# Kernel tuning notes

Hardware: AMD Instinct MI355X
Metric: run time of the kernel (lower is better)

Reference implementation:

```python
import jax, jax.numpy as jnp
import numpy as np

B, N, C, H, OUT = 4, 1024, 1024, 16, 1024
HEAD_DIM_INIT = C // H          # 64, used for scale per __init__
SCALE = HEAD_DIM_INIT ** -0.5
HD = 2 * C // H                 # 128, actual per-head dim after the reshape


def setup_inputs() -> dict:
    key = jax.random.key(0)
    k0, k1, k2, k3 = jax.random.split(key, 4)
    return {
        "x": jax.random.normal(k0, (B, N, C), jnp.float32),
        "context": jax.random.normal(k1, (B, N, C), jnp.float32),
        "w_qkv": jax.random.normal(k2, (3 * C, C), jnp.float32) / np.sqrt(C).astype(np.float32),
        "w_proj": jax.random.normal(k3, (OUT, C), jnp.float32) / np.sqrt(C).astype(np.float32),
        "b_proj": jnp.zeros((OUT,), jnp.float32),
    }


def reference(x, context, w_qkv, w_proj, b_proj):
    b, n, c = x.shape
    hd = 2 * c // H
    xc = jnp.concatenate([x, context], axis=1)                 # [B, 2N, C]
    qkv = jnp.einsum('bsc,dc->bsd', xc, w_qkv)                 # [B, 2N, 3C]
    # faithful to torch: reshape(B, N, 3, H, 2C/H) then permute(2,0,3,1,4)
    qkv = qkv.reshape(b, n, 3, H, hd).transpose(2, 0, 3, 1, 4)  # [3, B, H, N, HD]
    q, k, v = qkv[0], qkv[1], qkv[2]
    attn = jax.nn.softmax(jnp.einsum('bhqd,bhkd->bhqk', q, k) * SCALE, axis=-1)  # [B,H,N,N]
    o = jnp.einsum('bhqk,bhkd->bhqd', attn, v)                 # [B, H, N, HD]
    o = o.transpose(0, 2, 1, 3).reshape(b, 2 * n, c)           # [B, 2N, C]
    out = jnp.einsum('bsc,oc->bso', o, w_proj) + b_proj        # [B, 2N, OUT]
    return out, attn
```

## Files before the change

### kernel.cpp

```cpp
#include <hip/hip_runtime.h>
#include <stdint.h>

typedef short bf16x8 __attribute__((ext_vector_type(8)));
typedef short s16x4 __attribute__((ext_vector_type(4)));
typedef unsigned short us8 __attribute__((ext_vector_type(8)));
typedef float f32x4 __attribute__((ext_vector_type(4)));
typedef unsigned short u16;
typedef unsigned int u32;

__device__ __forceinline__ u16 f2bf(float f) {
    u32 u = __float_as_uint(f);
    return (u16)((u + 0x7FFFu + ((u >> 16) & 1u)) >> 16);
}
__device__ __forceinline__ float bf2f(u16 h) { return __uint_as_float(((u32)h) << 16); }

__device__ __forceinline__ u32 cvtpk(float lo, float hi) {
    u32 r;
    asm("v_cvt_pk_bf16_f32 %0, %1, %2" : "=v"(r) : "v"(lo), "v"(hi));
    return r;
}

typedef __attribute__((address_space(3))) unsigned int lds_uint;
typedef const __attribute__((address_space(1))) unsigned int glb_uint;
__device__ __forceinline__ void gld16(const void* g, void* l) {
    __builtin_amdgcn_global_load_lds((glb_uint*)g, (lds_uint*)l, 16, 0, 0);
}

#define VWAIT(n) asm volatile("s_waitcnt vmcnt(" #n ") lgkmcnt(0)" ::: "memory")
#define LWAIT    asm volatile("s_waitcnt lgkmcnt(0)" ::: "memory")
#define BARRIER  do { __builtin_amdgcn_s_barrier(); __builtin_amdgcn_sched_barrier(0); } while (0)


__device__ __forceinline__ void gld_p128x32(const u16* __restrict__ g, int64_t stride,
                                            u16* lds, int w, int lane) {
#pragma unroll
    for (int i = 0; i < 2; ++i) {
        const int grp = w * 2 + i;
        const int row = grp * 16 + (lane >> 2);
        const int sl = (lane & 3) ^ ((row >> 1) & 3);
        gld16(g + (int64_t)row * stride + (sl << 3), &lds[grp * 512]);
    }
}
__device__ __forceinline__ int idx128x32(int row, int gk) {
    return row * 32 + ((gk ^ ((row >> 1) & 3)) << 3);
}

__device__ __forceinline__ void gld_t32x128(const u16* __restrict__ g, int64_t stride,
                                            u16* lds, int w, int lane) {
#pragma unroll
    for (int i = 0; i < 2; ++i) {
        const int gg = w * 2 + i;
        const int row = gg * 4 + (lane >> 4);
        const int gs = (lane & 15) ^ (row & 7);
        gld16(g + (int64_t)row * stride + (gs << 3), &lds[gg * 512]);
    }
}
__device__ __forceinline__ void gld_t64x128(const u16* __restrict__ g, int64_t stride,
                                            u16* lds, int w, int lane) {
#pragma unroll
    for (int i = 0; i < 4; ++i) {
        const int gg = w * 4 + i;
        const int row = gg * 4 + (lane >> 4);
        const int gs = (lane & 15) ^ (row & 7);
        gld16(g + (int64_t)row * stride + (gs << 3), &lds[gg * 512]);
    }
}
__device__ __forceinline__ int idxT(int row, int gk) {
    return row * 128 + ((gk ^ (row & 7)) << 3);
}

__device__ __forceinline__ void gld_v128x64(const u16* __restrict__ g, int64_t stride,
                                            u16* lds, int w, int lane) {
#pragma unroll
    for (int i = 0; i < 4; ++i) {
        const int seg = w * 4 + i;
        const int row = seg * 8 + (lane >> 3);
        const int gs = (lane & 7) ^ (row & 7);
        gld16(g + (int64_t)row * stride + (gs << 3), &lds[seg * 512]);
    }
}
__device__ __forceinline__ int idxV(int row, int g3) {
    return row * 64 + ((g3 ^ (row & 7)) << 3);
}

__global__ void k0_all(const float* __restrict__ wqkv, const float* __restrict__ x,
                       const float* __restrict__ ctx, const float* __restrict__ wproj,
                       u16* __restrict__ Wh, u16* __restrict__ Xh,
                       u16* __restrict__ Phw) {
    const int gid = blockIdx.x;
    const float* src; u16* dst; int mode; int lg;
    if (gid < 1536)      { src = wqkv;  dst = Wh;  mode = 0; lg = gid; }
    else if (gid < 3584) { src = x;     dst = Xh;  mode = 1; lg = gid - 1536; }
    else if (gid < 5632) { src = ctx;   dst = Xh;  mode = 2; lg = gid - 3584; }
    else                 { src = wproj; dst = Phw; mode = 0; lg = gid - 5632; }
    const int64_t base = ((int64_t)lg * 256 + threadIdx.x) * 8;
    const int row = (int)(base >> 10), col = (int)(base & 1023);
    int orow = row;
    if (mode == 1) orow = row + ((row >> 10) << 10);
    else if (mode == 2) orow = row + (((row >> 10) + 1) << 10);
    const float4* sp = reinterpret_cast<const float4*>(src + base);
    float4 a = sp[0], b = sp[1];
    float v[8] = {a.x, a.y, a.z, a.w, b.x, b.y, b.z, b.w};
    us8 hh;
#pragma unroll
    for (int j = 0; j < 8; ++j) hh[j] = f2bf(v[j]);
    *reinterpret_cast<us8*>(&dst[(int64_t)orow * 1024 + col]) = hh;
}

template<bool ISK4>
__global__ __launch_bounds__(512, 1) void gemm8p(const u16* __restrict__ Ap,
                                                 const u16* __restrict__ Bp,
                                                 const float* __restrict__ bias,
                                                 u16* __restrict__ outh,
                                                 float* __restrict__ outf) {
    __shared__ u16 L[3][2][8192];
    const int tid = threadIdx.x, lane = tid & 63;
    const int w = tid >> 6, wm = w >> 2, wn = w & 3;
    const int rl = lane & 15, gk = lane >> 4, r4 = gk << 2;
    const int n0 = blockIdx.x << 7, m0 = blockIdx.y << 8;
    const u16* Ab = Ap + (int64_t)m0 * 1024;
    const u16* Bb = Bp + (int64_t)n0 * 1024;
    const int srow0 = tid >> 3, scol = tid & 7;
    f32x4 acc[2][4][2] = {};
    bf16x8 afr[4][2];

#define STAGE1(X, KT) do { if ((X) >= 0 && (KT) < 16) {                          \
    const u16* _b = (((X) < 2) ? (Ab + (int64_t)((X) * 128) * 1024) : Bb)        \
                    + (KT) * 64;                                                 \
    u16* _l = &L[((X) < 0) ? 0 : (X)][(KT) & 1][0];                              \
    _Pragma("unroll") for (int _j = 0; _j < 2; ++_j) {                           \
        const int _r = _j * 64 + srow0;                                          \
        const int _g = scol ^ (_r & 7);                                          \
        gld16(_b + (int64_t)_r * 1024 + _g * 8, &_l[_r * 64 + scol * 8]);        \
    } } } while (0)

#define RDF(X, PAR, ROW, KHGK)                                                   \
    (*reinterpret_cast<const bf16x8*>(                                           \
        &L[(X)][(PAR)][(ROW) * 64 + (((KHGK) ^ ((ROW) & 7)) << 3)]))

#define PHASE(QM, QN, PAR, STX, STKT, WMODE) do {                                \
    STAGE1(STX, STKT);                                                           \
    if ((WMODE) == 1) { VWAIT(4); } else if ((WMODE) == 2) { VWAIT(0); }         \
    __builtin_amdgcn_s_barrier(); __builtin_amdgcn_sched_barrier(0);             \
    if ((QN) == 0) {                                                             \
        _Pragma("unroll") for (int _mf = 0; _mf < 4; ++_mf) {                    \
            afr[_mf][0] = RDF(QM, PAR, wm * 64 + _mf * 16 + rl, gk);             \
            afr[_mf][1] = RDF(QM, PAR, wm * 64 + _mf * 16 + rl, 4 + gk);         \
        } }                                                                      \
    bf16x8 _b0 = RDF(2, PAR, (QN) * 64 + wn * 16 + rl, gk);                      \
    bf16x8 _b1 = RDF(2, PAR, (QN) * 64 + wn * 16 + rl, 4 + gk);                  \
    LWAIT; __builtin_amdgcn_sched_barrier(0);                                    \
    __builtin_amdgcn_s_setprio(1);                                               \
    _Pragma("unroll") for (int _mf = 0; _mf < 4; ++_mf) {                        \
        acc[QM][_mf][QN] = __builtin_amdgcn_mfma_f32_16x16x32_bf16(              \
            afr[_mf][0], _b0, acc[QM][_mf][QN], 0, 0, 0);                        \
        acc[QM][_mf][QN] = __builtin_amdgcn_mfma_f32_16x16x32_bf16(              \
            afr[_mf][1], _b1, acc[QM][_mf][QN], 0, 0, 0);                        \
    }                                                                            \
    __builtin_amdgcn_s_setprio(0);                                               \
    __builtin_amdgcn_s_barrier(); __builtin_amdgcn_sched_barrier(0);             \
} while (0)

    STAGE1(0, 0); STAGE1(1, 0); STAGE1(2, 0); STAGE1(0, 1);
    for (int i = 0; i < 8; ++i) {
        const int t = 2 * i;
        PHASE(0, 0, 0, 1, t + 1, 1);
        PHASE(0, 1, 0, 2, t + 1, 0);
        PHASE(1, 0, 0, 0, t + 2, 0);
        PHASE(1, 1, 0, -1, 0, 0);
        PHASE(0, 0, 1, 1, t + 2, (i == 7) ? 2 : 1);
        PHASE(0, 1, 1, 2, t + 2, 0);
        PHASE(1, 0, 1, 0, t + 3, 0);
        PHASE(1, 1, 1, -1, 0, 0);
    }
#undef PHASE
#undef RDF
#undef STAGE1
#pragma unroll
    for (int qm = 0; qm < 2; ++qm)
#pragma unroll
        for (int mf = 0; mf < 4; ++mf)
#pragma unroll
            for (int qn = 0; qn < 2; ++qn)
#pragma unroll
                for (int j = 0; j < 4; ++j) {
                    const int row = m0 + qm * 128 + wm * 64 + mf * 16 + r4 + j;
                    const int col = n0 + qn * 64 + wn * 16 + rl;
                    if (ISK4)
                        outf[(int64_t)row * 1024 + col] = acc[qm][mf][qn][j] + bias[col];
                    else
                        outh[(int64_t)row * 3072 + col] = f2bf(acc[qm][mf][qn][j]);
                }
}

__global__ __launch_bounds__(256, 2) void k0v_vt(const u16* __restrict__ Qh,
                                                 u16* __restrict__ Vt) {
    __shared__ u16 T[128][144];
    const int tid = threadIdx.x;
    const int z = blockIdx.y, b = z >> 4, h = z & 15;
    const int kt = blockIdx.x;
    const int c0v = (h < 8) ? (1024 + h * 128) : (2048 + (h - 8) * 128);
    const u16* Vbase = Qh + ((int64_t)b * 2048 + 1) * 3072 + c0v;
    const int row = tid >> 1, e0 = (tid & 1) << 6;
    const u16* src = Vbase + (int64_t)(kt * 128 + row) * 6144 + e0;
#pragma unroll
    for (int i = 0; i < 8; ++i) {
        us8 v = *reinterpret_cast<const us8*>(src + i * 8);
#pragma unroll
        for (int j = 0; j < 8; ++j) T[e0 + i * 8 + j][row] = v[j];
    }
    __syncthreads();
    const int e = tid >> 1, k0 = (tid & 1) << 6;
    u16* dst = Vt + ((int64_t)z << 17) + (int64_t)e * 1024 + kt * 128 + k0;
#pragma unroll
    for (int i = 0; i < 8; ++i)
        *reinterpret_cast<us8*>(dst + i * 8) = *reinterpret_cast<const us8*>(&T[e][k0 + i * 8]);
}

__global__ __launch_bounds__(256, 2) void k23_fused(const u16* __restrict__ Qh,
                                                    const u16* __restrict__ Vt,
                                                    float* __restrict__ attn,
                                                    u16* __restrict__ Obf) {
    __shared__ u16 LQ[4096];
    __shared__ u16 LKV[3][8192];
    __shared__ u16 Ph[32 * 72];
    __shared__ float pS[4][32];
    __shared__ float rowInv[32];
    const int tid = threadIdx.x, lane = tid & 63, w = tid >> 6;
    const u32 wgid = blockIdx.x;
    const int xcd = wgid & 7, t0 = wgid >> 3;
    const int mt = t0 & 31, z = ((t0 >> 5) << 3) + xcd;
    const int b = z >> 4, h = z & 15;
    const int m0 = mt << 5;
    const u16* Qbase = Qh + ((int64_t)b * 2048 + 2 * m0) * 3072 + h * 128;
    const int pk  = (h < 8) ? 0 : 1;
    const int c0k = (h < 8) ? (2048 + h * 128) : ((h - 8) * 128);
    const u16* Kbase = Qh + ((int64_t)b * 2048 + pk) * 3072 + c0k;
    const u16* Vtz = Vt + ((int64_t)z << 17);
    float* attnZ = attn + ((int64_t)z << 20) + (int64_t)m0 * 1024;
    const int rl = lane & 15, gk = lane >> 4;
    const int r4 = gk << 2;
    const int sm = w & 1, sn = w >> 1;
    gld_t32x128(Qbase, 6144, LQ, w, lane);
    gld_t64x128(Kbase,             6144, LKV[0], w, lane);
    gld_t64x128(Kbase + 64 * 6144, 6144, LKV[1], w, lane);
    u32 pk0[32], pk1[32];
    float ssum0 = 0.f, ssum1 = 0.f;
#pragma unroll
    for (int t = 0; t < 16; ++t) {
        if (t == 15) { VWAIT(0); } else { VWAIT(4); }
        BARRIER;
        if (t < 14)
            gld_t64x128(Kbase + (int64_t)(t + 2) * 64 * 6144, 6144, LKV[(t + 2) % 3], w, lane);
        f32x4 s0 = {}, s1 = {};
#pragma unroll
        for (int ks = 0; ks < 4; ++ks) {
            bf16x8 kf = *reinterpret_cast<const bf16x8*>(&LKV[t % 3][idxT(w * 16 + rl, ks * 4 + gk)]);
            bf16x8 q0 = *reinterpret_cast<const bf16x8*>(&LQ[idxT(rl, ks * 4 + gk)]);
            bf16x8 q1 = *reinterpret_cast<const bf16x8*>(&LQ[idxT(16 + rl, ks * 4 + gk)]);
            s0 = __builtin_amdgcn_mfma_f32_16x16x32_bf16(kf, q0, s0, 0, 0, 0);
            s1 = __builtin_amdgcn_mfma_f32_16x16x32_bf16(kf, q1, s1, 0, 0, 0);
        }
        float p0[4], p1[4];
#pragma unroll
        for (int j = 0; j < 4; ++j) {
            p0[j] = __expf(s0[j] * 0.125f); ssum0 += p0[j];
            p1[j] = __expf(s1[j] * 0.125f); ssum1 += p1[j];
        }
        pk0[2 * t]     = cvtpk(p0[0], p0[1]);
        pk1[2 * t]     = cvtpk(p0[2], p0[3]);
        pk0[2 * t + 1] = cvtpk(p1[0], p1[1]);
        pk1[2 * t + 1] = cvtpk(p1[2], p1[3]);
    }
    ssum0 += __shfl_xor(ssum0, 16); ssum0 += __shfl_xor(ssum0, 32);
    ssum1 += __shfl_xor(ssum1, 16); ssum1 += __shfl_xor(ssum1, 32);
    if (lane < 16) { pS[w][lane] = ssum0; pS[w][16 + lane] = ssum1; }
    LWAIT; BARRIER;
    gld_v128x64(Vtz,      1024, LKV[0], w, lane);
    gld_v128x64(Vtz + 64, 1024, LKV[1], w, lane);
    if (tid < 32)
        rowInv[tid] = 1.0f / (pS[0][tid] + pS[1][tid] + pS[2][tid] + pS[3][tid]);
    LWAIT; BARRIER;
    const float Iq0 = rowInv[rl], Iq1 = rowInv[16 + rl];
    float IqO[4];
#pragma unroll
    for (int j = 0; j < 4; ++j) IqO[j] = rowInv[sm * 16 + r4 + j];
    f32x4 po[4] = {};
#pragma unroll
    for (int t = 0; t < 16; ++t) {
        if (t == 0)       { VWAIT(4); }
        else if (t == 15) { VWAIT(2); }
        else              { VWAIT(6); }
        BARRIER;
        if (t < 14)
            gld_v128x64(Vtz + (t + 2) * 64, 1024, LKV[(t + 2) % 3], w, lane);
        const u32 a0 = pk0[2 * t], a1 = pk1[2 * t];
        const u32 b0 = pk0[2 * t + 1], b1 = pk1[2 * t + 1];
        *reinterpret_cast<uint2*>(&Ph[rl * 72 + w * 16 + r4])        = make_uint2(a0, a1);
        *reinterpret_cast<uint2*>(&Ph[(16 + rl) * 72 + w * 16 + r4]) = make_uint2(b0, b1);
        *reinterpret_cast<float4*>(&attnZ[(int64_t)rl * 1024 + t * 64 + w * 16 + r4])
            = make_float4(__uint_as_float(a0 << 16) * Iq0,
                          __uint_as_float(a0 & 0xFFFF0000u) * Iq0,
                          __uint_as_float(a1 << 16) * Iq0,
                          __uint_as_float(a1 & 0xFFFF0000u) * Iq0);
        *reinterpret_cast<float4*>(&attnZ[(int64_t)(16 + rl) * 1024 + t * 64 + w * 16 + r4])
            = make_float4(__uint_as_float(b0 << 16) * Iq1,
                          __uint_as_float(b0 & 0xFFFF0000u) * Iq1,
                          __uint_as_float(b1 << 16) * Iq1,
                          __uint_as_float(b1 & 0xFFFF0000u) * Iq1);
        LWAIT; BARRIER;
        bf16x8 pa0 = *reinterpret_cast<const bf16x8*>(&Ph[(sm * 16 + rl) * 72 + gk * 8]);
        bf16x8 pa1 = *reinterpret_cast<const bf16x8*>(&Ph[(sm * 16 + rl) * 72 + 32 + gk * 8]);
#pragma unroll
        for (int n = 0; n < 4; ++n) {
            bf16x8 bv0 = *reinterpret_cast<const bf16x8*>(&LKV[t % 3][idxV(sn * 64 + n * 16 + rl, gk)]);
            bf16x8 bv1 = *reinterpret_cast<const bf16x8*>(&LKV[t % 3][idxV(sn * 64 + n * 16 + rl, 4 + gk)]);
            po[n] = __builtin_amdgcn_mfma_f32_16x16x32_bf16(pa0, bv0, po[n], 0, 0, 0);
            po[n] = __builtin_amdgcn_mfma_f32_16x16x32_bf16(pa1, bv1, po[n], 0, 0, 0);
        }
    }
    const int poh = h >> 3, cb2 = (h & 7) << 7;
#pragma unroll
    for (int n = 0; n < 4; ++n)
#pragma unroll
        for (int j = 0; j < 4; ++j) {
            const int qrow = m0 + sm * 16 + r4 + j;
            Obf[((int64_t)b * 2048 + 2 * qrow + poh) * 1024
                + cb2 + sn * 64 + n * 16 + rl] = f2bf(po[n][j] * IqO[j]);
        }
}

extern "C" void kernel_launch(void* const* d_in, const int* in_sizes, int n_in,
                              void* d_out, int out_size, void* d_ws, size_t ws_size,
                              hipStream_t stream) {
    const float* x     = (const float*)d_in[0];
    const float* ctx   = (const float*)d_in[1];
    const float* wqkv  = (const float*)d_in[2];
    const float* wproj = (const float*)d_in[3];
    const float* bias  = (const float*)d_in[4];
    float* out  = (float*)d_out;
    float* attn = out + 8388608;

    u16* Qh  = (u16*)d_ws;
    u16* Vt  = Qh + 25165824;
    u16* Wh  = Vt + 8388608;
    u16* Phw = Wh + 3145728;
    u16* Obf = Phw + 1048576;

    u16* Xh = (u16*)attn;

    k0_all        <<<dim3(6144),   256, 0, stream>>>(wqkv, x, ctx, wproj, Wh, Xh, Phw);
    gemm8p<false> <<<dim3(24, 32), 512, 0, stream>>>(Xh, Wh, nullptr, Qh, nullptr);
    k0v_vt        <<<dim3(8, 64),  256, 0, stream>>>(Qh, Vt);
    k23_fused     <<<dim3(2048),   256, 0, stream>>>(Qh, Vt, attn, Obf);
    gemm8p<true>  <<<dim3(8, 32),  512, 0, stream>>>(Obf, Phw, bias, nullptr, out);
}
```

Measured before the change: 231.8 us.

## Double attention query tile to 64 rows with 8-wave workgroups sharing K/V tiles

The fused attention kernel now processes 64 query rows per workgroup with 512 threads (8 waves) instead of 32 rows with 4 waves, halving the grid. Each K and V tile staged in LDS is reused by twice as many query rows, which cuts global/L2 traffic for K and V, and the per-wave async load count and wait counts are adjusted to match. In exchange, LDS use per workgroup grows and launch_bounds(512,4) may constrain registers, which matters because of the 64 packed probability registers each thread keeps.

```diff
diff --git a/kernel.cpp b/kernel.cpp
--- a/kernel.cpp
+++ b/kernel.cpp
@@ -2,7 +2,6 @@
 #include <stdint.h>
 
 typedef short bf16x8 __attribute__((ext_vector_type(8)));
-typedef short s16x4 __attribute__((ext_vector_type(4)));
 typedef unsigned short us8 __attribute__((ext_vector_type(8)));
 typedef float f32x4 __attribute__((ext_vector_type(4)));
 typedef unsigned short u16;
@@ -12,7 +11,6 @@
     u32 u = __float_as_uint(f);
     return (u16)((u + 0x7FFFu + ((u >> 16) & 1u)) >> 16);
 }
-__device__ __forceinline__ float bf2f(u16 h) { return __uint_as_float(((u32)h) << 16); }
 
 __device__ __forceinline__ u32 cvtpk(float lo, float hi) {
     u32 r;
@@ -31,22 +29,8 @@
 #define BARRIER  do { __builtin_amdgcn_s_barrier(); __builtin_amdgcn_sched_barrier(0); } while (0)
 
 
-__device__ __forceinline__ void gld_p128x32(const u16* __restrict__ g, int64_t stride,
-                                            u16* lds, int w, int lane) {
-#pragma unroll
-    for (int i = 0; i < 2; ++i) {
-        const int grp = w * 2 + i;
-        const int row = grp * 16 + (lane >> 2);
-        const int sl = (lane & 3) ^ ((row >> 1) & 3);
-        gld16(g + (int64_t)row * stride + (sl << 3), &lds[grp * 512]);
-    }
-}
-__device__ __forceinline__ int idx128x32(int row, int gk) {
-    return row * 32 + ((gk ^ ((row >> 1) & 3)) << 3);
-}
-
-__device__ __forceinline__ void gld_t32x128(const u16* __restrict__ g, int64_t stride,
-                                            u16* lds, int w, int lane) {
+__device__ __forceinline__ void gld8_t64x128(const u16* __restrict__ g, int64_t stride,
+                                             u16* lds, int w, int lane) {
 #pragma unroll
     for (int i = 0; i < 2; ++i) {
         const int gg = w * 2 + i;
@@ -55,25 +39,15 @@
         gld16(g + (int64_t)row * stride + (gs << 3), &lds[gg * 512]);
     }
 }
-__device__ __forceinline__ void gld_t64x128(const u16* __restrict__ g, int64_t stride,
-                                            u16* lds, int w, int lane) {
-#pragma unroll
-    for (int i = 0; i < 4; ++i) {
-        const int gg = w * 4 + i;
-        const int row = gg * 4 + (lane >> 4);
-        const int gs = (lane & 15) ^ (row & 7);
-        gld16(g + (int64_t)row * stride + (gs << 3), &lds[gg * 512]);
-    }
-}
 __device__ __forceinline__ int idxT(int row, int gk) {
     return row * 128 + ((gk ^ (row & 7)) << 3);
 }
 
-__device__ __forceinline__ void gld_v128x64(const u16* __restrict__ g, int64_t stride,
-                                            u16* lds, int w, int lane) {
-#pragma unroll
-    for (int i = 0; i < 4; ++i) {
-        const int seg = w * 4 + i;
+__device__ __forceinline__ void gld8_v128x64(const u16* __restrict__ g, int64_t stride,
+                                             u16* lds, int w, int lane) {
+#pragma unroll
+    for (int i = 0; i < 2; ++i) {
+        const int seg = w * 2 + i;
         const int row = seg * 8 + (lane >> 3);
         const int gs = (lane & 7) ^ (row & 7);
         gld16(g + (int64_t)row * stride + (gs << 3), &lds[seg * 512]);
@@ -217,47 +191,47 @@
         *reinterpret_cast<us8*>(dst + i * 8) = *reinterpret_cast<const us8*>(&T[e][k0 + i * 8]);
 }
 
-__global__ __launch_bounds__(256, 2) void k23_fused(const u16* __restrict__ Qh,
+__global__ __launch_bounds__(512, 4) void k23_fused(const u16* __restrict__ Qh,
                                                     const u16* __restrict__ Vt,
                                                     float* __restrict__ attn,
                                                     u16* __restrict__ Obf) {
-    __shared__ u16 LQ[4096];
+    __shared__ u16 LQ[8192];
     __shared__ u16 LKV[3][8192];
-    __shared__ u16 Ph[32 * 72];
-    __shared__ float pS[4][32];
-    __shared__ float rowInv[32];
+    __shared__ u16 Ph[64 * 72];
+    __shared__ float pS[8][32];
+    __shared__ float rowInv[64];
     const int tid = threadIdx.x, lane = tid & 63, w = tid >> 6;
     const u32 wgid = blockIdx.x;
     const int xcd = wgid & 7, t0 = wgid >> 3;
-    const int mt = t0 & 31, z = ((t0 >> 5) << 3) + xcd;
+    const int mt = t0 & 15, z = ((t0 >> 4) << 3) + xcd;
     const int b = z >> 4, h = z & 15;
-    const int m0 = mt << 5;
+    const int m0 = mt << 6;
+    const int kt = w & 3, qh = w >> 2;
+    const int qq = w & 3, sv = w >> 2;
+    const int rl = lane & 15, gk = lane >> 4, r4 = gk << 2;
     const u16* Qbase = Qh + ((int64_t)b * 2048 + 2 * m0) * 3072 + h * 128;
     const int pk  = (h < 8) ? 0 : 1;
     const int c0k = (h < 8) ? (2048 + h * 128) : ((h - 8) * 128);
     const u16* Kbase = Qh + ((int64_t)b * 2048 + pk) * 3072 + c0k;
     const u16* Vtz = Vt + ((int64_t)z << 17);
     float* attnZ = attn + ((int64_t)z << 20) + (int64_t)m0 * 1024;
-    const int rl = lane & 15, gk = lane >> 4;
-    const int r4 = gk << 2;
-    const int sm = w & 1, sn = w >> 1;
-    gld_t32x128(Qbase, 6144, LQ, w, lane);
-    gld_t64x128(Kbase,             6144, LKV[0], w, lane);
-    gld_t64x128(Kbase + 64 * 6144, 6144, LKV[1], w, lane);
+    gld8_t64x128(Qbase, 6144, LQ, w, lane);
+    gld8_t64x128(Kbase,             6144, LKV[0], w, lane);
+    gld8_t64x128(Kbase + 64 * 6144, 6144, LKV[1], w, lane);
     u32 pk0[32], pk1[32];
     float ssum0 = 0.f, ssum1 = 0.f;
 #pragma unroll
     for (int t = 0; t < 16; ++t) {
-        if (t == 15) { VWAIT(0); } else { VWAIT(4); }
+        if (t == 15) { VWAIT(0); } else { VWAIT(2); }
         BARRIER;
         if (t < 14)
-            gld_t64x128(Kbase + (int64_t)(t + 2) * 64 * 6144, 6144, LKV[(t + 2) % 3], w, lane);
+            gld8_t64x128(Kbase + (int64_t)(t + 2) * 64 * 6144, 6144, LKV[(t + 2) % 3], w, lane);
         f32x4 s0 = {}, s1 = {};
 #pragma unroll
         for (int ks = 0; ks < 4; ++ks) {
-            bf16x8 kf = *reinterpret_cast<const bf16x8*>(&LKV[t % 3][idxT(w * 16 + rl, ks * 4 + gk)]);
-            bf16x8 q0 = *reinterpret_cast<const bf16x8*>(&LQ[idxT(rl, ks * 4 + gk)]);
-            bf16x8 q1 = *reinterpret_cast<const bf16x8*>(&LQ[idxT(16 + rl, ks * 4 + gk)]);
+            bf16x8 kf = *reinterpret_cast<const bf16x8*>(&LKV[t % 3][idxT(kt * 16 + rl, ks * 4 + gk)]);
+            bf16x8 q0 = *reinterpret_cast<const bf16x8*>(&LQ[idxT(qh * 32 + rl, ks * 4 + gk)]);
+            bf16x8 q1 = *reinterpret_cast<const bf16x8*>(&LQ[idxT(qh * 32 + 16 + rl, ks * 4 + gk)]);
             s0 = __builtin_amdgcn_mfma_f32_16x16x32_bf16(kf, q0, s0, 0, 0, 0);
             s1 = __builtin_amdgcn_mfma_f32_16x16x32_bf16(kf, q1, s1, 0, 0, 0);
         }
@@ -276,45 +250,51 @@
     ssum1 += __shfl_xor(ssum1, 16); ssum1 += __shfl_xor(ssum1, 32);
     if (lane < 16) { pS[w][lane] = ssum0; pS[w][16 + lane] = ssum1; }
     LWAIT; BARRIER;
-    gld_v128x64(Vtz,      1024, LKV[0], w, lane);
-    gld_v128x64(Vtz + 64, 1024, LKV[1], w, lane);
-    if (tid < 32)
-        rowInv[tid] = 1.0f / (pS[0][tid] + pS[1][tid] + pS[2][tid] + pS[3][tid]);
+    gld8_v128x64(Vtz,      1024, LKV[0], w, lane);
+    gld8_v128x64(Vtz + 64, 1024, LKV[1], w, lane);
+    if (tid < 64) {
+        const int qb = (tid >> 5) << 2;
+        rowInv[tid] = 1.0f / (pS[qb][tid & 31] + pS[qb + 1][tid & 31]
+                              + pS[qb + 2][tid & 31] + pS[qb + 3][tid & 31]);
+    }
     LWAIT; BARRIER;
-    const float Iq0 = rowInv[rl], Iq1 = rowInv[16 + rl];
+    const float Iq0 = rowInv[qh * 32 + rl], Iq1 = rowInv[qh * 32 + 16 + rl];
     float IqO[4];
 #pragma unroll
-    for (int j = 0; j < 4; ++j) IqO[j] = rowInv[sm * 16 + r4 + j];
+    for (int j = 0; j < 4; ++j) IqO[j] = rowInv[qq * 16 + r4 + j];
     f32x4 po[4] = {};
 #pragma unroll
     for (int t = 0; t < 16; ++t) {
-        if (t == 0)       { VWAIT(4); }
-        else if (t == 15) { VWAIT(2); }
+        if (t == 0)       { VWAIT(2); }
+        else if (t == 1)  { VWAIT(4); }
+        else if (t == 15) { VWAIT(4); }
         else              { VWAIT(6); }
         BARRIER;
         if (t < 14)
-            gld_v128x64(Vtz + (t + 2) * 64, 1024, LKV[(t + 2) % 3], w, lane);
+            gld8_v128x64(Vtz + (t + 2) * 64, 1024, LKV[(t + 2) % 3], w, lane);
         const u32 a0 = pk0[2 * t], a1 = pk1[2 * t];
         const u32 b0 = pk0[2 * t + 1], b1 = pk1[2 * t + 1];
-        *reinterpret_cast<uint2*>(&Ph[rl * 72 + w * 16 + r4])        = make_uint2(a0, a1);
-        *reinterpret_cast<uint2*>(&Ph[(16 + rl) * 72 + w * 16 + r4]) = make_uint2(b0, b1);
-        *reinterpret_cast<float4*>(&attnZ[(int64_t)rl * 1024 + t * 64 + w * 16 + r4])
+        *reinterpret_cast<uint2*>(&Ph[(qh * 32 + rl) * 72 + kt * 16 + r4])
+            = make_uint2(a0, a1);
+        *reinterpret_cast<uint2*>(&Ph[(qh * 32 + 16 + rl) * 72 + kt * 16 + r4])
+            = make_uint2(b0, b1);
+        *reinterpret_cast<float4*>(&attnZ[(int64_t)(qh * 32 + rl) * 1024 + t * 64 + kt * 16 + r4])
             = make_float4(__uint_as_float(a0 << 16) * Iq0,
                           __uint_as_float(a0 & 0xFFFF0000u) * Iq0,
                           __uint_as_float(a1 << 16) * Iq0,
                           __uint_as_float(a1 & 0xFFFF0000u) * Iq0);
-        *reinterpret_cast<float4*>(&attnZ[(int64_t)(16 + rl) * 1024 + t * 64 + w * 16 + r4])
+        *reinterpret_cast<float4*>(&attnZ[(int64_t)(qh * 32 + 16 + rl) * 1024 + t * 64 + kt * 16 + r4])
             = make_float4(__uint_as_float(b0 << 16) * Iq1,
                           __uint_as_float(b0 & 0xFFFF0000u) * Iq1,
                           __uint_as_float(b1 << 16) * Iq1,
                           __uint_as_float(b1 & 0xFFFF0000u) * Iq1);
         LWAIT; BARRIER;
-        bf16x8 pa0 = *reinterpret_cast<const bf16x8*>(&Ph[(sm * 16 + rl) * 72 + gk * 8]);
-        bf16x8 pa1 = *reinterpret_cast<const bf16x8*>(&Ph[(sm * 16 + rl) * 72 + 32 + gk * 8]);
+        bf16x8 pa0 = *reinterpret_cast<const bf16x8*>(&Ph[(qq * 16 + rl) * 72 + gk * 8]);
+        bf16x8 pa1 = *reinterpret_cast<const bf16x8*>(&Ph[(qq * 16 + rl) * 72 + 32 + gk * 8]);
 #pragma unroll
         for (int n = 0; n < 4; ++n) {
-            bf16x8 bv0 = *reinterpret_cast<const bf16x8*>(&LKV[t % 3][idxV(sn * 64 + n * 16 + rl, gk)]);
-            bf16x8 bv1 = *reinterpret_cast<const bf16x8*>(&LKV[t % 3][idxV(sn * 64 + n * 16 + rl, 4 + gk)]);
+            bf16x8 bv0 = *reinterpret_cast<const bf16x8*>(&LKV[t % 3][idxV(sv * 64 + n * 16 + rl, gk)]);
+            bf16x8 bv1 = *reinterpret_cast<const bf16x8*>(&LKV[t % 3][idxV(sv * 64 + n * 16 + rl, 4 + gk)]);
             po[n] = __builtin_amdgcn_mfma_f32_16x16x32_bf16(pa0, bv0, po[n], 0, 0, 0);
             po[n] = __builtin_amdgcn_mfma_f32_16x16x32_bf16(pa1, bv1, po[n], 0, 0, 0);
         }
@@ -324,9 +304,9 @@
     for (int n = 0; n < 4; ++n)
 #pragma unroll
         for (int j = 0; j < 4; ++j) {
-            const int qrow = m0 + sm * 16 + r4 + j;
+            const int qrow = m0 + qq * 16 + r4 + j;
             Obf[((int64_t)b * 2048 + 2 * qrow + poh) * 1024
-                + cb2 + sn * 64 + n * 16 + rl] = f2bf(po[n][j] * IqO[j]);
+                + cb2 + sv * 64 + n * 16 + rl] = f2bf(po[n][j] * IqO[j]);
         }
 }
 
@@ -352,6 +332,6 @@
     k0_all        <<<dim3(6144),   256, 0, stream>>>(wqkv, x, ctx, wproj, Wh, Xh, Phw);
     gemm8p<false> <<<dim3(24, 32), 512, 0, stream>>>(Xh, Wh, nullptr, Qh, nullptr);
     k0v_vt        <<<dim3(8, 64),  256, 0, stream>>>(Qh, Vt);
-    k23_fused     <<<dim3(2048),   256, 0, stream>>>(Qh, Vt, attn, Obf);
+    k23_fused     <<<dim3(1024),   512, 0, stream>>>(Qh, Vt, attn, Obf);
     gemm8p<true>  <<<dim3(8, 32),  512, 0, stream>>>(Obf, Phw, bias, nullptr, out);
 }
```

Measured after the change: 204.9 us. 1.13x faster.
